# Kernel optimization log

Hardware: AMD Instinct MI355X
Metric: run time of the kernel (lower is better)

Reference implementation:

```python
import jax, jax.numpy as jnp
import numpy as np

B, S, D = 4, 4096, 512      # batch, seq_len, data_embedding_size
FH = 2048                    # forecasting_hidden_size
H = 64                       # lstm_hidden_size (proj_size=1 since H>1)


def setup_inputs() -> dict:
    key = jax.random.key(0)
    ks = jax.random.split(key, 10)
    sD, sFH, sH = 1.0 / np.sqrt(D), 1.0 / np.sqrt(FH), 1.0 / np.sqrt(H)
    return {
        "x": jax.random.normal(ks[0], (B, S, D), dtype=jnp.float32),
        # forecasting head: Linear(D->FH) then Linear(FH->D)
        "W1": jax.random.uniform(ks[1], (FH, D), minval=-sD, maxval=sD),
        "b1": jax.random.uniform(ks[2], (FH,), minval=-sD, maxval=sD),
        "W2": jax.random.uniform(ks[3], (D, FH), minval=-sFH, maxval=sFH),
        "b2": jax.random.uniform(ks[4], (D,), minval=-sFH, maxval=sFH),
        # LSTM (1 layer, proj_size=1): gate order i,f,g,o
        "Wih": jax.random.uniform(ks[5], (4 * H, D), minval=-sH, maxval=sH),
        "Whh": jax.random.uniform(ks[6], (4 * H, 1), minval=-sH, maxval=sH),  # recurrent input is projected h (size 1)
        "bih": jax.random.uniform(ks[7], (4 * H,), minval=-sH, maxval=sH),
        "bhh": jax.random.uniform(ks[8], (4 * H,), minval=-sH, maxval=sH),
        "Whr": jax.random.uniform(ks[9], (1, H), minval=-sH, maxval=sH),  # projection h_inner -> h
    }


def reference(x, W1, b1, W2, b2, Wih, Whh, bih, bhh, Whr):
    Bx, Sx, Dx = x.shape
    flat = x.reshape(-1, Dx)                       # [B*S, D]
    fore = (flat @ W1.T + b1) @ W2.T + b2          # [B*S, D]  (two linears, no activation)

    # Original code loops i in range(S) over the FLATTENED sequence -> only first S tokens.
    xs = flat[:Sx]
    fs = fore[:Sx]

    def cell(h, c, inp):
        # gates = W_ih x + b_ih + W_hh h + b_hh ; PyTorch order i,f,g,o
        g = Wih @ inp + bih + Whh @ h + bhh        # [4H]
        i, f, gg, o = jnp.split(g, 4)
        c2 = jax.nn.sigmoid(f) * c + jax.nn.sigmoid(i) * jnp.tanh(gg)
        h2 = Whr @ (jax.nn.sigmoid(o) * jnp.tanh(c2))   # projected hidden, shape [1]
        return h2, c2

    def step(carry, tok):
        h, c = carry
        xt, ft = tok
        h2, c2 = cell(h, c, xt)        # real token: updates state
        hf, _ = cell(h2, c2, ft)       # forecasted token: peeks, does not update state
        return (h2, c2), (h2[0], hf[0])

    init = (jnp.zeros((1,), x.dtype), jnp.zeros((H,), x.dtype))
    _, (p, pf) = jax.lax.scan(step, init, (xs, fs))   # p, pf: [S]

    progress = jnp.broadcast_to(p[None, :], (Bx, Sx))
    forecasted_progress = jnp.broadcast_to(pf[None, :], (Bx, Sx))
    return progress, forecasted_progress, fore.reshape(1, -1, Dx)
```

## Files before the change

kernel.cpp:

```cpp
#include <hip/hip_runtime.h>
#include <hip/hip_bf16.h>


#if __has_builtin(__builtin_amdgcn_exp2f)
__device__ __forceinline__ float EXP2(float x) { return __builtin_amdgcn_exp2f(x); }
#else
__device__ __forceinline__ float EXP2(float x) { return __expf(x * 0.6931471805599453f); }
#endif
#if __has_builtin(__builtin_amdgcn_rcpf)
__device__ __forceinline__ float RCPF(float x) { return __builtin_amdgcn_rcpf(x); }
#else
__device__ __forceinline__ float RCPF(float x) { return 1.0f / x; }
#endif

constexpr float L2E  = 1.4426950408889634f;
constexpr float L2E2 = 2.8853900817779268f;

__device__ __forceinline__ float fsig(float x) { return 1.0f / (1.0f + __expf(-x)); }
__device__ __forceinline__ float ftanh(float x) { return 1.0f - 2.0f / (1.0f + __expf(2.0f * x)); }
__device__ __forceinline__ float sig_f(float x)  { return RCPF(1.0f + EXP2(-L2E * x)); }
__device__ __forceinline__ float tanh_f(float x) { return fmaf(-2.0f, RCPF(1.0f + EXP2(L2E2 * x)), 1.0f); }

template<int CTRL>
__device__ __forceinline__ float dppadd(float x) {
    return x + __int_as_float(__builtin_amdgcn_update_dpp(
        0, __float_as_int(x), CTRL, 0xf, 0xf, true));
}
__device__ __forceinline__ float dpp_sum64_lane63(float x) {
    x = dppadd<0x111>(x); x = dppadd<0x112>(x); x = dppadd<0x114>(x);
    x = dppadd<0x118>(x); x = dppadd<0x142>(x); x = dppadd<0x143>(x);
    return x;
}
__device__ __forceinline__ float readlane63(float x) {
    return __int_as_float(__builtin_amdgcn_readlane(__float_as_int(x), 63));
}
__device__ __forceinline__ float readlane_s(float x, int s) {
    return __int_as_float(__builtin_amdgcn_readlane(__float_as_int(x), s));
}

using bf16x8 = __attribute__((ext_vector_type(8))) __bf16;
using f32x4  = __attribute__((ext_vector_type(4))) float;

__device__ __forceinline__ void mfma_tile128_lds(
    const __hip_bfloat16* __restrict__ A, int lda,
    const __hip_bfloat16* __restrict__ B, int ldb,
    int K, int bm, int bn,
    const float* __restrict__ bias,
    float* __restrict__ Cf, int ldc,
    __hip_bfloat16* __restrict__ Cb,
    __hip_bfloat16* __restrict__ Ct, int ldt,
    __hip_bfloat16* __restrict__ Bs)
{
    const int tid  = threadIdx.x;
    const int w    = tid >> 6;
    const int lane = tid & 63;
    const int rc   = lane & 15;
    const int kg   = lane >> 4;
    const __hip_bfloat16* ap0 = A + (size_t)(bm + w * 16 + rc) * lda + kg * 8;
    const __hip_bfloat16* ap1 = ap0 + (size_t)64 * lda;

#define LD8(P) (*reinterpret_cast<const bf16x8*>(P))
    const f32x4 z{0.f, 0.f, 0.f, 0.f};
    f32x4 c00 = z, c01 = z, c02 = z, c03 = z;
    f32x4 c10 = z, c11 = z, c12 = z, c13 = z;

    for (int kb = 0; kb < K; kb += 512) {
        __syncthreads();
        #pragma unroll
        for (int i = 0; i < 16; ++i) {
            const int G = i * 256 + tid;
            const int row = G >> 6, kc = G & 63;
            const bf16x8 v = LD8(B + (size_t)(bn + row) * ldb + kb + kc * 8);
            *reinterpret_cast<bf16x8*>(Bs + row * 512 + ((kc ^ (row & 7)) << 3)) = v;
        }
        __syncthreads();

        bf16x8 a0 = LD8(ap0 + kb), a1 = LD8(ap1 + kb);
        #pragma unroll 4
        for (int s = 0; s < 16; ++s) {
            bf16x8 a0n = a0, a1n = a1;
            if (s < 15) {
                a0n = LD8(ap0 + kb + (s + 1) * 32);
                a1n = LD8(ap1 + kb + (s + 1) * 32);
            }
            bf16x8 bf[4];
            #pragma unroll
            for (int g = 0; g < 4; ++g) {
                const int row = g * 16 + rc;
                const int off = row * 512 + (((s * 4 + kg) ^ (row & 7)) << 3);
                bf[g] = *reinterpret_cast<const bf16x8*>(Bs + off);
            }
            c00 = __builtin_amdgcn_mfma_f32_16x16x32_bf16(a0, bf[0], c00, 0, 0, 0);
            c01 = __builtin_amdgcn_mfma_f32_16x16x32_bf16(a0, bf[1], c01, 0, 0, 0);
            c02 = __builtin_amdgcn_mfma_f32_16x16x32_bf16(a0, bf[2], c02, 0, 0, 0);
            c03 = __builtin_amdgcn_mfma_f32_16x16x32_bf16(a0, bf[3], c03, 0, 0, 0);
            c10 = __builtin_amdgcn_mfma_f32_16x16x32_bf16(a1, bf[0], c10, 0, 0, 0);
            c11 = __builtin_amdgcn_mfma_f32_16x16x32_bf16(a1, bf[1], c11, 0, 0, 0);
            c12 = __builtin_amdgcn_mfma_f32_16x16x32_bf16(a1, bf[2], c12, 0, 0, 0);
            c13 = __builtin_amdgcn_mfma_f32_16x16x32_bf16(a1, bf[3], c13, 0, 0, 0);
            a0 = a0n; a1 = a1n;
        }
    }
#undef LD8

    const int row0 = bm + w * 16 + kg * 4;
    const int colb = bn + rc;
#define EPI(ACC, HOFF, CT) {                                                  \
        const int col = colb + (CT) * 16;                                     \
        const float bb = bias ? bias[col] : 0.0f;                             \
        _Pragma("unroll")                                                     \
        for (int i = 0; i < 4; ++i) {                                         \
            const float v = (ACC)[i] + bb;                                    \
            const int row = row0 + (HOFF) + i;                                \
            if (Cf) Cf[(size_t)row * ldc + col] = v;                          \
            if (Cb) Cb[(size_t)row * ldc + col] = __float2bfloat16(v);        \
            if (Ct) Ct[(size_t)col * ldt + row] = __float2bfloat16(v);        \
        }}
    EPI(c00, 0, 0)  EPI(c01, 0, 1)  EPI(c02, 0, 2)  EPI(c03, 0, 3)
    EPI(c10, 64, 0) EPI(c11, 64, 1) EPI(c12, 64, 2) EPI(c13, 64, 3)
#undef EPI
}

__global__ __launch_bounds__(256) void conv_kernel(
    const float* __restrict__ x, const float* __restrict__ W2,
    const float* __restrict__ W1, const float* __restrict__ Wih,
    const float* __restrict__ bih, const float* __restrict__ bhh,
    __hip_bfloat16* __restrict__ xb, __hip_bfloat16* __restrict__ W2b,
    __hip_bfloat16* __restrict__ Wihb, __hip_bfloat16* __restrict__ W1t,
    float* __restrict__ gxbias)
{
    const int bid = blockIdx.x, tid = threadIdx.x;
#define CVT4(SRC, DST, BASE) {                                                \
        const size_t i = ((size_t)(BASE) * 256 + tid) * 4;                    \
        const float4 v = *reinterpret_cast<const float4*>((SRC) + i);         \
        __hip_bfloat16 o[4] = {__float2bfloat16(v.x), __float2bfloat16(v.y),  \
                               __float2bfloat16(v.z), __float2bfloat16(v.w)}; \
        *reinterpret_cast<ushort4*>((DST) + i) =                              \
            *reinterpret_cast<const ushort4*>(o); }
    if (bid < 8192) {
        CVT4(x, xb, bid)
    } else if (bid < 9216) {
        CVT4(W2, W2b, bid - 8192)
    } else if (bid < 9344) {
        CVT4(Wih, Wihb, bid - 9216)
    } else if (bid < 9600) {
        __shared__ float lds[64][65];
        const int b = bid - 9344;
        const int br = b >> 3, bc = b & 7;
        const int r0 = tid >> 4, c4 = (tid & 15) * 4;
        #pragma unroll
        for (int u = 0; u < 4; ++u) {
            const int row = r0 + u * 16;
            const float4 v = *reinterpret_cast<const float4*>(
                &W1[(size_t)(br * 64 + row) * 512 + bc * 64 + c4]);
            lds[row][c4 + 0] = v.x; lds[row][c4 + 1] = v.y;
            lds[row][c4 + 2] = v.z; lds[row][c4 + 3] = v.w;
        }
        __syncthreads();
        const int jj0 = tid >> 4, kk4 = (tid & 15) * 4;
        #pragma unroll
        for (int u = 0; u < 4; ++u) {
            const int jj = jj0 + u * 16;
            __hip_bfloat16 o[4] = {
                __float2bfloat16(lds[kk4 + 0][jj]), __float2bfloat16(lds[kk4 + 1][jj]),
                __float2bfloat16(lds[kk4 + 2][jj]), __float2bfloat16(lds[kk4 + 3][jj])};
            *reinterpret_cast<ushort4*>(
                &W1t[(size_t)(bc * 64 + jj) * 2048 + br * 64 + kk4]) =
                *reinterpret_cast<const ushort4*>(o);
        }
    } else {
        gxbias[tid] = bih[tid] + bhh[tid];
    }
#undef CVT4
}

__global__ __launch_bounds__(256) void prep_kernel(
    const float* __restrict__ W2, const float* __restrict__ b1,
    const float* __restrict__ b2,
    const __hip_bfloat16* __restrict__ W2b, const __hip_bfloat16* __restrict__ W1t,
    const __hip_bfloat16* __restrict__ xb, const __hip_bfloat16* __restrict__ Wihb,
    const float* __restrict__ gxbias,
    __hip_bfloat16* __restrict__ Weffb, __hip_bfloat16* __restrict__ WeffTb,
    float* __restrict__ beff, float* __restrict__ Gx)
{
    __shared__ __hip_bfloat16 Bs[64 * 512];
    const int bid = blockIdx.x;
    if (bid < 32) {
        const int bm = (bid >> 3) * 128, bn = (bid & 7) * 64;
        mfma_tile128_lds(W2b, 2048, W1t, 2048, 2048, bm, bn, nullptr,
                         nullptr, 512, Weffb, WeffTb, 512, Bs);
    } else if (bid < 40) {
        const int w = threadIdx.x >> 6, j = threadIdx.x & 63;
        const int base = (bid - 32) * 64 + w * 16;
        for (int o = 0; o < 16; ++o) {
            const int i = base + o;
            float s = 0.0f;
            #pragma unroll
            for (int m = 0; m < 32; ++m)
                s = fmaf(W2[(size_t)i * 2048 + j + 64 * m], b1[j + 64 * m], s);
            s = dpp_sum64_lane63(s);
            if (j == 63) beff[i] = s + b2[i];
        }
    } else {
        const int b = bid - 40;
        const int bm = (b >> 2) * 128, bn = (b & 3) * 64;
        mfma_tile128_lds(xb, 512, Wihb, 512, 512, bm, bn, gxbias,
                         Gx, 256, nullptr, nullptr, 0, Bs);
    }
}

__global__ __launch_bounds__(256) void wg_kernel(
    const __hip_bfloat16* __restrict__ Wihb, const __hip_bfloat16* __restrict__ WeffTb,
    const float* __restrict__ Wih, const float* __restrict__ beff,
    __hip_bfloat16* __restrict__ Wgb, float* __restrict__ bf2)
{
    __shared__ __hip_bfloat16 Bs[64 * 512];
    const int bid = blockIdx.x;
    if (bid < 16) {
        const int bm = (bid >> 3) * 128, bn = (bid & 7) * 64;
        mfma_tile128_lds(Wihb, 512, WeffTb, 512, 512, bm, bn, nullptr,
                         nullptr, 512, Wgb, nullptr, 0, Bs);
    } else {
        const int w = threadIdx.x >> 6, j = threadIdx.x & 63;
        for (int o = 0; o < 64; ++o) {
            const int i = w * 64 + o;
            float s = 0.0f;
            #pragma unroll
            for (int m = 0; m < 8; ++m)
                s = fmaf(Wih[(size_t)i * 512 + j + 64 * m], beff[j + 64 * m], s);
            s = dpp_sum64_lane63(s);
            if (j == 63) bf2[i] = s;
        }
    }
}

__global__ __launch_bounds__(256) void fused_kernel(
    int phase, int first, int last,
    int fore_cnt, int gf_cnt,
    const __hip_bfloat16* __restrict__ xb, const __hip_bfloat16* __restrict__ Weffb,
    const __hip_bfloat16* __restrict__ Wgb,
    const float* __restrict__ beff, const float* __restrict__ bf2,
    const float* __restrict__ Gx,
    const float* __restrict__ Whh, const float* __restrict__ Whr,
    const float* __restrict__ hprev, float* __restrict__ hnext,
    float* __restrict__ P, float* __restrict__ Q,
    float* __restrict__ c_hist, float* __restrict__ p,
    float* __restrict__ fore, float* __restrict__ Gf)
{
    __shared__ __hip_bfloat16 Bs[64 * 512];
    constexpr int CH = 32;

    if (blockIdx.x < 32) {
        const int chunk = blockIdx.x * 4 + (threadIdx.x >> 6);
        const int j = threadIdx.x & 63;
        const float wi = Whh[j], wf = Whh[64 + j];
        const float wg2 = Whh[128 + j], wo = Whh[192 + j];
        const float* ab = Gx + (size_t)chunk * CH * 256 + j;

        float hp = 0.0f;
        if (!first) {
            const int idx = chunk * CH - 1 + j;
            hp = (idx >= 0 && idx < 4096) ? hprev[idx] : 0.0f;
        }

        if (phase == 0) {
            float Pv = 1.0f, Qv = 0.0f;
            #pragma unroll 8
            for (int s = 0; s < CH; ++s) {
                const float hs = first ? 0.0f : readlane_s(hp, s);
                const float ai = ab[s * 256]       + wi  * hs;
                const float af = ab[s * 256 + 64]  + wf  * hs;
                const float ag = ab[s * 256 + 128] + wg2 * hs;
                const float si = sig_f(ai);
                const float sf = sig_f(af);
                const float tg = tanh_f(ag);
                Pv = sf * Pv;
                Qv = fmaf(sf, Qv, si * tg);
            }
            P[chunk * 64 + j] = Pv;
            Q[chunk * 64 + j] = Qv;
        } else {
            const float whr = Whr[j];
            float c = 0.0f;
            #pragma unroll 8
            for (int m = 0; m < chunk; ++m)
                c = fmaf(P[m * 64 + j], c, Q[m * 64 + j]);
            float vp = 0.0f;
            #pragma unroll 4
            for (int s = 0; s < CH; ++s) {
                const float hs = first ? 0.0f : readlane_s(hp, s);
                const float ai = ab[s * 256]       + wi  * hs;
                const float af = ab[s * 256 + 64]  + wf  * hs;
                const float ag = ab[s * 256 + 128] + wg2 * hs;
                const float ao = ab[s * 256 + 192] + wo  * hs;
                const float si = sig_f(ai);
                const float sf = sig_f(af);
                const float tg = tanh_f(ag);
                const float so = sig_f(ao);
                c = fmaf(sf, c, si * tg);
                if (last) c_hist[(size_t)(chunk * CH + s) * 64 + j] = c;
                const float tc = tanh_f(c);
                float hv = tc * (so * whr);
                hv = dpp_sum64_lane63(hv);
                const float hn = readlane63(hv);
                vp = (j == s) ? hn : vp;
            }
            if (j < CH) {
                hnext[chunk * CH + j] = vp;
                if (last) p[chunk * CH + j] = vp;
            }
        }
        return;
    }

    const int bt = blockIdx.x - 32;
    if (bt < fore_cnt) {
        const int bm = (bt >> 3) * 128, bn = (bt & 7) * 64;
        mfma_tile128_lds(xb, 512, Weffb, 512, 512, bm, bn, beff,
                         fore, 512, nullptr, nullptr, 0, Bs);
    } else if (bt < fore_cnt + gf_cnt) {
        const int g = bt - fore_cnt;
        const int bm = (g >> 2) * 128, bn = (g & 3) * 64;
        mfma_tile128_lds(xb, 512, Wgb, 512, 512, bm, bn, bf2,
                         Gf, 256, nullptr, nullptr, 0, Bs);
    }
}

__global__ __launch_bounds__(256) void finish_kernel(
    const float* __restrict__ Gf,
    const float* __restrict__ Whh, const float* __restrict__ bih,
    const float* __restrict__ bhh, const float* __restrict__ Whr,
    const float* __restrict__ c_hist, const float* __restrict__ p,
    float* __restrict__ out)
{
    constexpr int S = 4096, BS = 4 * 4096;
    const int bid = blockIdx.x;
    if (bid < 64) {
        const int w = threadIdx.x >> 6, j = threadIdx.x & 63;
        const float bi0 = bih[j]       + bhh[j];
        const float bi1 = bih[64 + j]  + bhh[64 + j];
        const float bi2 = bih[128 + j] + bhh[128 + j];
        const float bi3 = bih[192 + j] + bhh[192 + j];
        for (int o = 0; o < 16; ++o) {
            const int t = bid * 64 + w * 16 + o;
            const float h2 = p[t];
            const float c2 = c_hist[(size_t)t * 64 + j];
            const float* G = Gf + (size_t)t * 256;
            const float gi = G[j]       + bi0 + Whh[j] * h2;
            const float gf = G[64 + j]  + bi1 + Whh[64 + j] * h2;
            const float gg = G[128 + j] + bi2 + Whh[128 + j] * h2;
            const float go = G[192 + j] + bi3 + Whh[192 + j] * h2;
            const float cf = fsig(gf) * c2 + fsig(gi) * ftanh(gg);
            float hv = fsig(go) * ftanh(cf) * Whr[j];
            hv = dpp_sum64_lane63(hv);
            if (j == 63) {
                out[BS + 0 * S + t] = hv;
                out[BS + 1 * S + t] = hv;
                out[BS + 2 * S + t] = hv;
                out[BS + 3 * S + t] = hv;
            }
        }
    } else {
        const int i = (bid - 64) * 256 + threadIdx.x;
        out[i] = p[i & (S - 1)];
    }
}

extern "C" void kernel_launch(void* const* d_in, const int* in_sizes, int n_in,
                              void* d_out, int out_size, void* d_ws, size_t ws_size,
                              hipStream_t stream) {
    const float* x   = (const float*)d_in[0];
    const float* W1  = (const float*)d_in[1];
    const float* b1  = (const float*)d_in[2];
    const float* W2  = (const float*)d_in[3];
    const float* b2  = (const float*)d_in[4];
    const float* Wih = (const float*)d_in[5];
    const float* Whh = (const float*)d_in[6];
    const float* bih = (const float*)d_in[7];
    const float* bhh = (const float*)d_in[8];
    const float* Whr = (const float*)d_in[9];
    float* out = (float*)d_out;

    constexpr int Bb = 4, S = 4096;
    const int M = Bb * S;

    float* ws      = (float*)d_ws;
    float* beff    = ws;
    float* gxbias  = beff + 512;
    float* bf2     = gxbias + 256;
    float* Gx      = bf2 + 256;
    float* Gf      = Gx + S * 256;
    float* c_hist  = Gf + S * 256;
    float* p       = c_hist + S * 64;
    float* Pp      = p + S;
    float* Qq      = Pp + 8192;
    float* h0      = Qq + 8192;
    float* h1      = h0 + S;
    __hip_bfloat16* xb     = (__hip_bfloat16*)(h1 + S);
    __hip_bfloat16* W2b    = xb + (size_t)M * 512;
    __hip_bfloat16* W1t    = W2b + 512 * 2048;
    __hip_bfloat16* Wihb   = W1t + 512 * 2048;
    __hip_bfloat16* Weffb  = Wihb + 256 * 512;
    __hip_bfloat16* WeffTb = Weffb + 512 * 512;
    __hip_bfloat16* Wgb    = WeffTb + 512 * 512;

    float* fore = out + 2 * M;

    conv_kernel<<<9601, 256, 0, stream>>>(
        x, W2, W1, Wih, bih, bhh, xb, W2b, Wihb, W1t, gxbias);

    prep_kernel<<<168, 256, 0, stream>>>(
        W2, b1, b2, W2b, W1t, xb, Wihb, gxbias, Weffb, WeffTb, beff, Gx);

    wg_kernel<<<17, 256, 0, stream>>>(Wihb, WeffTb, Wih, beff, Wgb, bf2);

    fused_kernel<<<32 + 1024, 256, 0, stream>>>(
        0, 1, 0, 1024, 0, xb, Weffb, Wgb, beff, bf2, Gx, Whh, Whr,
        h0, h0, Pp, Qq, c_hist, p, fore, Gf);
    fused_kernel<<<32 + 128, 256, 0, stream>>>(
        1, 1, 0, 0, 128, xb, Weffb, Wgb, beff, bf2, Gx, Whh, Whr,
        h0, h0, Pp, Qq, c_hist, p, fore, Gf);
    fused_kernel<<<32, 256, 0, stream>>>(
        0, 0, 0, 0, 0, xb, Weffb, Wgb, beff, bf2, Gx, Whh, Whr,
        h0, h1, Pp, Qq, c_hist, p, fore, Gf);
    fused_kernel<<<32, 256, 0, stream>>>(
        1, 0, 1, 0, 0, xb, Weffb, Wgb, beff, bf2, Gx, Whh, Whr,
        h0, h1, Pp, Qq, c_hist, p, fore, Gf);

    finish_kernel<<<128, 256, 0, stream>>>(
        Gf, Whh, bih, bhh, Whr, c_hist, p, out);
}
```

Before: 162.4 us.

## Fold wg and finish kernels into fused recurrence launches and swizzle tile order

The separate Wg/bf2 precompute kernel now runs as extra blocks in the first fused launch, next to the forecast GEMM. The finish kernel is removed: the last recurrence pass computes the forecasted-token peek step inline and writes both progress outputs directly. This drops the c_hist round trip and two launches. GEMM block-to-tile mapping is also swizzled for better cache locality, but the serial last pass now carries more per-step work.

```diff
diff --git a/kernel.cpp b/kernel.cpp
--- a/kernel.cpp
+++ b/kernel.cpp
@@ -16,8 +16,6 @@
 constexpr float L2E  = 1.4426950408889634f;
 constexpr float L2E2 = 2.8853900817779268f;
 
-__device__ __forceinline__ float fsig(float x) { return 1.0f / (1.0f + __expf(-x)); }
-__device__ __forceinline__ float ftanh(float x) { return 1.0f - 2.0f / (1.0f + __expf(2.0f * x)); }
 __device__ __forceinline__ float sig_f(float x)  { return RCPF(1.0f + EXP2(-L2E * x)); }
 __device__ __forceinline__ float tanh_f(float x) { return fmaf(-2.0f, RCPF(1.0f + EXP2(L2E2 * x)), 1.0f); }
 
@@ -203,52 +201,31 @@
         }
     } else {
         const int b = bid - 40;
-        const int bm = (b >> 2) * 128, bn = (b & 3) * 64;
+        const int tile = (b & 7) * 16 + (b >> 3);
+        const int bm = (tile >> 2) * 128, bn = (tile & 3) * 64;
         mfma_tile128_lds(xb, 512, Wihb, 512, 512, bm, bn, gxbias,
                          Gx, 256, nullptr, nullptr, 0, Bs);
     }
 }
 
-__global__ __launch_bounds__(256) void wg_kernel(
-    const __hip_bfloat16* __restrict__ Wihb, const __hip_bfloat16* __restrict__ WeffTb,
-    const float* __restrict__ Wih, const float* __restrict__ beff,
-    __hip_bfloat16* __restrict__ Wgb, float* __restrict__ bf2)
-{
-    __shared__ __hip_bfloat16 Bs[64 * 512];
-    const int bid = blockIdx.x;
-    if (bid < 16) {
-        const int bm = (bid >> 3) * 128, bn = (bid & 7) * 64;
-        mfma_tile128_lds(Wihb, 512, WeffTb, 512, 512, bm, bn, nullptr,
-                         nullptr, 512, Wgb, nullptr, 0, Bs);
-    } else {
-        const int w = threadIdx.x >> 6, j = threadIdx.x & 63;
-        for (int o = 0; o < 64; ++o) {
-            const int i = w * 64 + o;
-            float s = 0.0f;
-            #pragma unroll
-            for (int m = 0; m < 8; ++m)
-                s = fmaf(Wih[(size_t)i * 512 + j + 64 * m], beff[j + 64 * m], s);
-            s = dpp_sum64_lane63(s);
-            if (j == 63) bf2[i] = s;
-        }
-    }
-}
-
 __global__ __launch_bounds__(256) void fused_kernel(
     int phase, int first, int last,
-    int fore_cnt, int gf_cnt,
+    int fore_cnt, int gf_cnt, int wg_cnt,
     const __hip_bfloat16* __restrict__ xb, const __hip_bfloat16* __restrict__ Weffb,
-    const __hip_bfloat16* __restrict__ Wgb,
-    const float* __restrict__ beff, const float* __restrict__ bf2,
-    const float* __restrict__ Gx,
+    const __hip_bfloat16* __restrict__ WeffTb, const __hip_bfloat16* __restrict__ Wihb,
+    __hip_bfloat16* __restrict__ Wgb, const __hip_bfloat16* __restrict__ Wgb_in,
+    const float* __restrict__ Wih, const float* __restrict__ beff,
+    float* __restrict__ bf2_out, const float* __restrict__ bf2,
+    const float* __restrict__ Gx, float* __restrict__ Gf,
+    const float* __restrict__ Gf_in, const float* __restrict__ gxbias,
     const float* __restrict__ Whh, const float* __restrict__ Whr,
     const float* __restrict__ hprev, float* __restrict__ hnext,
     float* __restrict__ P, float* __restrict__ Q,
-    float* __restrict__ c_hist, float* __restrict__ p,
-    float* __restrict__ fore, float* __restrict__ Gf)
+    float* __restrict__ fore, float* __restrict__ out)
 {
     __shared__ __hip_bfloat16 Bs[64 * 512];
     constexpr int CH = 32;
+    constexpr int S = 4096, BS = 4 * 4096;
 
     if (blockIdx.x < 32) {
         const int chunk = blockIdx.x * 4 + (threadIdx.x >> 6);
@@ -260,7 +237,7 @@
         float hp = 0.0f;
         if (!first) {
             const int idx = chunk * CH - 1 + j;
-            hp = (idx >= 0 && idx < 4096) ? hprev[idx] : 0.0f;
+            hp = (idx >= 0 && idx < S) ? hprev[idx] : 0.0f;
         }
 
         if (phase == 0) {
@@ -285,7 +262,10 @@
             #pragma unroll 8
             for (int m = 0; m < chunk; ++m)
                 c = fmaf(P[m * 64 + j], c, Q[m * 64 + j]);
-            float vp = 0.0f;
+            float vp = 0.0f, vpf = 0.0f;
+            const float* gfp = Gf_in ? Gf_in + (size_t)chunk * CH * 256 + j : nullptr;
+            const float bi0 = gxbias[j],        bi1 = gxbias[64 + j];
+            const float bi2 = gxbias[128 + j],  bi3 = gxbias[192 + j];
             #pragma unroll 4
             for (int s = 0; s < CH; ++s) {
                 const float hs = first ? 0.0f : readlane_s(hp, s);
@@ -298,16 +278,34 @@
                 const float tg = tanh_f(ag);
                 const float so = sig_f(ao);
                 c = fmaf(sf, c, si * tg);
-                if (last) c_hist[(size_t)(chunk * CH + s) * 64 + j] = c;
                 const float tc = tanh_f(c);
                 float hv = tc * (so * whr);
                 hv = dpp_sum64_lane63(hv);
                 const float hn = readlane63(hv);
                 vp = (j == s) ? hn : vp;
+                if (last) {
+                    const float fi = gfp[s * 256]       + bi0 + wi  * hn;
+                    const float ff = gfp[s * 256 + 64]  + bi1 + wf  * hn;
+                    const float fg = gfp[s * 256 + 128] + bi2 + wg2 * hn;
+                    const float fo = gfp[s * 256 + 192] + bi3 + wo  * hn;
+                    const float cf = sig_f(ff) * c + sig_f(fi) * tanh_f(fg);
+                    float hf = sig_f(fo) * tanh_f(cf) * whr;
+                    hf = dpp_sum64_lane63(hf);
+                    const float hfn = readlane63(hf);
+                    vpf = (j == s) ? hfn : vpf;
+                }
             }
             if (j < CH) {
-                hnext[chunk * CH + j] = vp;
-                if (last) p[chunk * CH + j] = vp;
+                const int t = chunk * CH + j;
+                if (last) {
+                    #pragma unroll
+                    for (int b = 0; b < 4; ++b) {
+                        out[b * S + t]      = vp;
+                        out[BS + b * S + t] = vpf;
+                    }
+                } else {
+                    hnext[t] = vp;
+                }
             }
         }
         return;
@@ -315,54 +313,34 @@
 
     const int bt = blockIdx.x - 32;
     if (bt < fore_cnt) {
-        const int bm = (bt >> 3) * 128, bn = (bt & 7) * 64;
+        const int tile = (bt & 7) * 128 + (bt >> 3);
+        const int bm = (tile >> 3) * 128, bn = (tile & 7) * 64;
         mfma_tile128_lds(xb, 512, Weffb, 512, 512, bm, bn, beff,
                          fore, 512, nullptr, nullptr, 0, Bs);
     } else if (bt < fore_cnt + gf_cnt) {
         const int g = bt - fore_cnt;
-        const int bm = (g >> 2) * 128, bn = (g & 3) * 64;
-        mfma_tile128_lds(xb, 512, Wgb, 512, 512, bm, bn, bf2,
+        const int tile = (g & 7) * 16 + (g >> 3);
+        const int bm = (tile >> 2) * 128, bn = (tile & 3) * 64;
+        mfma_tile128_lds(xb, 512, Wgb_in, 512, 512, bm, bn, bf2,
                          Gf, 256, nullptr, nullptr, 0, Bs);
-    }
-}
-
-__global__ __launch_bounds__(256) void finish_kernel(
-    const float* __restrict__ Gf,
-    const float* __restrict__ Whh, const float* __restrict__ bih,
-    const float* __restrict__ bhh, const float* __restrict__ Whr,
-    const float* __restrict__ c_hist, const float* __restrict__ p,
-    float* __restrict__ out)
-{
-    constexpr int S = 4096, BS = 4 * 4096;
-    const int bid = blockIdx.x;
-    if (bid < 64) {
-        const int w = threadIdx.x >> 6, j = threadIdx.x & 63;
-        const float bi0 = bih[j]       + bhh[j];
-        const float bi1 = bih[64 + j]  + bhh[64 + j];
-        const float bi2 = bih[128 + j] + bhh[128 + j];
-        const float bi3 = bih[192 + j] + bhh[192 + j];
-        for (int o = 0; o < 16; ++o) {
-            const int t = bid * 64 + w * 16 + o;
-            const float h2 = p[t];
-            const float c2 = c_hist[(size_t)t * 64 + j];
-            const float* G = Gf + (size_t)t * 256;
-            const float gi = G[j]       + bi0 + Whh[j] * h2;
-            const float gf = G[64 + j]  + bi1 + Whh[64 + j] * h2;
-            const float gg = G[128 + j] + bi2 + Whh[128 + j] * h2;
-            const float go = G[192 + j] + bi3 + Whh[192 + j] * h2;
-            const float cf = fsig(gf) * c2 + fsig(gi) * ftanh(gg);
-            float hv = fsig(go) * ftanh(cf) * Whr[j];
-            hv = dpp_sum64_lane63(hv);
-            if (j == 63) {
-                out[BS + 0 * S + t] = hv;
-                out[BS + 1 * S + t] = hv;
-                out[BS + 2 * S + t] = hv;
-                out[BS + 3 * S + t] = hv;
-            }
-        }
-    } else {
-        const int i = (bid - 64) * 256 + threadIdx.x;
-        out[i] = p[i & (S - 1)];
+    } else if (bt < fore_cnt + gf_cnt + wg_cnt) {
+        const int t = bt - fore_cnt - gf_cnt;
+        if (t < 16) {
+            const int bm = (t >> 3) * 128, bn = (t & 7) * 64;
+            mfma_tile128_lds(Wihb, 512, WeffTb, 512, 512, bm, bn, nullptr,
+                             nullptr, 512, Wgb, nullptr, 0, Bs);
+        } else {
+            const int w = threadIdx.x >> 6, j = threadIdx.x & 63;
+            for (int o = 0; o < 64; ++o) {
+                const int i = w * 64 + o;
+                float s = 0.0f;
+                #pragma unroll
+                for (int m = 0; m < 8; ++m)
+                    s = fmaf(Wih[(size_t)i * 512 + j + 64 * m], beff[j + 64 * m], s);
+                s = dpp_sum64_lane63(s);
+                if (j == 63) bf2_out[i] = s;
+            }
+        }
     }
 }
 
@@ -390,9 +368,7 @@
     float* bf2     = gxbias + 256;
     float* Gx      = bf2 + 256;
     float* Gf      = Gx + S * 256;
-    float* c_hist  = Gf + S * 256;
-    float* p       = c_hist + S * 64;
-    float* Pp      = p + S;
+    float* Pp      = Gf + S * 256;
     float* Qq      = Pp + 8192;
     float* h0      = Qq + 8192;
     float* h1      = h0 + S;
@@ -412,21 +388,27 @@
     prep_kernel<<<168, 256, 0, stream>>>(
         W2, b1, b2, W2b, W1t, xb, Wihb, gxbias, Weffb, WeffTb, beff, Gx);
 
-    wg_kernel<<<17, 256, 0, stream>>>(Wihb, WeffTb, Wih, beff, Wgb, bf2);
-
-    fused_kernel<<<32 + 1024, 256, 0, stream>>>(
-        0, 1, 0, 1024, 0, xb, Weffb, Wgb, beff, bf2, Gx, Whh, Whr,
-        h0, h0, Pp, Qq, c_hist, p, fore, Gf);
+    fused_kernel<<<32 + 1024 + 17, 256, 0, stream>>>(
+        0, 1, 0, 1024, 0, 17,
+        xb, Weffb, WeffTb, Wihb, Wgb, Wgb, Wih, beff, bf2, bf2,
+        Gx, Gf, nullptr, gxbias, Whh, Whr,
+        h0, h0, Pp, Qq, fore, out);
+
     fused_kernel<<<32 + 128, 256, 0, stream>>>(
-        1, 1, 0, 0, 128, xb, Weffb, Wgb, beff, bf2, Gx, Whh, Whr,
-        h0, h0, Pp, Qq, c_hist, p, fore, Gf);
+        1, 1, 0, 0, 128, 0,
+        xb, Weffb, WeffTb, Wihb, Wgb, Wgb, Wih, beff, bf2, bf2,
+        Gx, Gf, nullptr, gxbias, Whh, Whr,
+        h0, h0, Pp, Qq, fore, out);
+
     fused_kernel<<<32, 256, 0, stream>>>(
-        0, 0, 0, 0, 0, xb, Weffb, Wgb, beff, bf2, Gx, Whh, Whr,
-        h0, h1, Pp, Qq, c_hist, p, fore, Gf);
+        0, 0, 0, 0, 0, 0,
+        xb, Weffb, WeffTb, Wihb, Wgb, Wgb, Wih, beff, bf2, bf2,
+        Gx, Gf, nullptr, gxbias, Whh, Whr,
+        h0, h1, Pp, Qq, fore, out);
+
     fused_kernel<<<32, 256, 0, stream>>>(
-        1, 0, 1, 0, 0, xb, Weffb, Wgb, beff, bf2, Gx, Whh, Whr,
-        h0, h1, Pp, Qq, c_hist, p, fore, Gf);
-
-    finish_kernel<<<128, 256, 0, stream>>>(
-        Gf, Whh, bih, bhh, Whr, c_hist, p, out);
-}
+        1, 0, 1, 0, 0, 0,
+        xb, Weffb, WeffTb, Wihb, Wgb, Wgb, Wih, beff, bf2, bf2,
+        Gx, Gf, Gf, gxbias, Whh, Whr,
+        h0, h1, Pp, Qq, fore, out);
+}
```

Measured after the change: 151.5 us. -6.7%, faster.
